# Performance work log

Measured on AMD Instinct MI355X. Metric: run time of the kernel, lower is better.

## Reference

```python
import jax, jax.numpy as jnp
import numpy as np

B, C, H, W = 4, 256, 128, 128
HEADS, KD, VD = 8, 64, 64
EPS = 1e-5


def setup_inputs() -> dict:
    key = jax.random.key(0)
    ks = jax.random.split(key, 5)
    s = 0.02
    return {
        "x": jax.random.normal(ks[0], (B, C, H, W), dtype=jnp.float32),
        "wq": jax.random.normal(ks[1], (HEADS * KD, C), dtype=jnp.float32) * s,
        "bq": jnp.zeros((HEADS * KD,), dtype=jnp.float32),
        "wk": jax.random.normal(ks[2], (HEADS * KD, C), dtype=jnp.float32) * s,
        "bk": jnp.zeros((HEADS * KD,), dtype=jnp.float32),
        "wv": jax.random.normal(ks[3], (HEADS * VD, C), dtype=jnp.float32) * s,
        "bv": jnp.zeros((HEADS * VD,), dtype=jnp.float32),
        "wo": jax.random.normal(ks[4], (C, HEADS * VD), dtype=jnp.float32) * s,
        "bo": jnp.zeros((C,), dtype=jnp.float32),
        "g_q": jnp.ones((KD,), dtype=jnp.float32),
        "be_q": jnp.zeros((KD,), dtype=jnp.float32),
        "g_k": jnp.ones((KD,), dtype=jnp.float32),
        "be_k": jnp.zeros((KD,), dtype=jnp.float32),
        "g_v": jnp.ones((VD,), dtype=jnp.float32),
        "be_v": jnp.zeros((VD,), dtype=jnp.float32),
    }


def _conv1x1(t, w, b):
    # t: [B,C,H,W], w: [O,C] -> [B,O,H,W]
    return jnp.einsum("bchw,oc->bohw", t, w) + b[None, :, None, None]


def _ln_dim(t, g, be):
    # LayerNorm over the per-head feature axis (axis=2) of [B,heads,dim,N]
    mu = jnp.mean(t, axis=2, keepdims=True)
    var = jnp.var(t, axis=2, keepdims=True)
    return (t - mu) * jax.lax.rsqrt(var + EPS) * g[None, None, :, None] + be[None, None, :, None]


def reference(x, wq, bq, wk, bk, wv, bv, wo, bo, g_q, be_q, g_k, be_k, g_v, be_v):
    b, c, h, w = x.shape
    n = h * w
    # context defaults to x
    q = _conv1x1(x, wq, bq).reshape(b, HEADS, KD, n)
    k = _conv1x1(x, wk, bk).reshape(b, HEADS, KD, n)
    v = _conv1x1(x, wv, bv).reshape(b, HEADS, VD, n)
    q = _ln_dim(q, g_q, be_q)
    k = _ln_dim(k, g_k, be_k)
    v = _ln_dim(v, g_v, be_v)
    q = jax.nn.softmax(q * (KD ** -0.25), axis=2)  # softmax over key_dim
    k = jax.nn.softmax(k, axis=3)                  # softmax over N
    ctx = jnp.einsum("bhkn,bhvn->bhkv", k, v)      # [B,heads,KD,VD]
    out = jnp.einsum("bhkn,bhkv->bhvn", q, ctx)    # [B,heads,VD,N]
    out = out.reshape(b, HEADS * VD, h, w)
    return _conv1x1(out, wo, bo)
```

## Files before the change

### kernel.cpp

```cpp
#include <hip/hip_runtime.h>
#include <hip/hip_bf16.h>
#include <stdint.h>

typedef unsigned short u16;
typedef __attribute__((__vector_size__(16))) short s16x8;
typedef __attribute__((__vector_size__(16))) float f32x4;

#define N_ 16384
#define C_ 256

__device__ __forceinline__ float bf2f(u16 u) {
    union { uint32_t i; float f; } v; v.i = ((uint32_t)u) << 16; return v.f;
}
__device__ __forceinline__ u16 f2bf(float f) {
    union { uint32_t i; float f; } v; v.f = f;
    uint32_t u = v.i;
    return (u16)((u + 0x7FFFu + ((u >> 16) & 1u)) >> 16);
}

__device__ __forceinline__ void gl_lds16(const u16* g, u16* l) {
    __builtin_amdgcn_global_load_lds((__attribute__((address_space(1))) void*)g,
                                     (__attribute__((address_space(3))) void*)l,
                                     16, 0, 0);
}

__global__ __launch_bounds__(256) void zero_kernel(float* __restrict__ p, int n) {
    int i = blockIdx.x * 256 + threadIdx.x;
    if (i < n) p[i] = 0.f;
}

__global__ __launch_bounds__(256) void transpose_kernel(const float* __restrict__ x,
                                                        u16* __restrict__ xT) {
    __shared__ float T[64][65];
    int tid = threadIdx.x;
    int n0 = blockIdx.x * 64, c0 = blockIdx.y * 64, b = blockIdx.z;
    const float* xp = x + (size_t)b * C_ * N_;
    for (int it = 0; it < 16; it++) {
        int idx = it * 256 + tid;
        int c = idx >> 6, n = idx & 63;
        T[c][n] = xp[(size_t)(c0 + c) * N_ + n0 + n];
    }
    __syncthreads();
    u16* op = xT + (size_t)b * N_ * C_;
    for (int it = 0; it < 8; it++) {
        int idx = it * 256 + tid;
        int n = idx >> 5, c2 = (idx & 31) * 2;
        uint32_t lo = f2bf(T[c2][n]);
        uint32_t hi = f2bf(T[c2 + 1][n]);
        *(uint32_t*)&op[(size_t)(n0 + n) * C_ + c0 + c2] = lo | (hi << 16);
    }
}

__global__ __launch_bounds__(256) void cvtw_kernel(const float* __restrict__ wq,
                                                   const float* __restrict__ wk,
                                                   const float* __restrict__ wv,
                                                   u16* __restrict__ wb) {
    int m = blockIdx.y;
    const float* s = m == 0 ? wq : (m == 1 ? wk : wv);
    int i = blockIdx.x * 256 + threadIdx.x;
    wb[(size_t)m * 131072 + i] = f2bf(s[i]);
}


__global__ __launch_bounds__(256) void kv_kernel(
    const u16* __restrict__ xT, const u16* __restrict__ wb,
    const float* __restrict__ bk, const float* __restrict__ bv,
    const float* __restrict__ gk, const float* __restrict__ bek,
    const float* __restrict__ gv, const float* __restrict__ bev,
    u16* __restrict__ eKb, u16* __restrict__ vbb, float* __restrict__ rs)
{
    __shared__ u16 WS[128 * 64];
    __shared__ u16 XS[128 * 64];
    int tid = threadIdx.x;
    int lane = tid & 63, wid = tid >> 6;
    int quad = lane >> 4, l15 = lane & 15;
    int wm = wid >> 1, wn = wid & 1;
    int bx = blockIdx.x, sec = blockIdx.y, b = blockIdx.z;
    int kind2 = sec >> 2, pair = sec & 3;
    int r0 = pair * 128;
    int n0 = bx * 128;

    const float* bptr  = kind2 ? bv  : bk;
    const float* gptr  = kind2 ? gv  : gk;
    const float* beptr = kind2 ? bev : bek;
    const u16* wsrc = wb + (size_t)(1 + kind2) * 131072 + (size_t)r0 * 256;
    const u16* xsrc = xT + ((size_t)b * N_ + n0) * 256;

    f32x4 acc[4][4];
#pragma unroll
    for (int i = 0; i < 4; i++)
#pragma unroll
        for (int j = 0; j < 4; j++) acc[i][j] = (f32x4){0.f, 0.f, 0.f, 0.f};

    int srow = lane >> 3;
    int sc8  = ((lane & 7) ^ srow) * 8;

    for (int kc = 0; kc < 4; kc++) {
        int koff = kc * 64 + sc8;
#pragma unroll
        for (int i = 0; i < 4; i++) {
            int row = (wid * 4 + i) * 8 + srow;
            gl_lds16(&wsrc[(size_t)row * 256 + koff], &WS[(wid * 4 + i) * 512]);
            gl_lds16(&xsrc[(size_t)row * 256 + koff], &XS[(wid * 4 + i) * 512]);
        }
        __syncthreads();
#pragma unroll
        for (int ks = 0; ks < 2; ks++) {
            int cc = ks * 4 + quad;
            s16x8 af[4], bf[4];
#pragma unroll
            for (int f = 0; f < 4; f++) {
                int ar = wn * 64 + f * 16 + l15;
                int br = wm * 64 + f * 16 + l15;
                af[f] = *(const s16x8*)&XS[ar * 64 + ((cc ^ (ar & 7)) * 8)];
                bf[f] = *(const s16x8*)&WS[br * 64 + ((cc ^ (br & 7)) * 8)];
            }
#pragma unroll
            for (int i = 0; i < 4; i++)
#pragma unroll
                for (int j = 0; j < 4; j++)
                    acc[i][j] = __builtin_amdgcn_mfma_f32_16x16x32_bf16(af[i], bf[j], acc[i][j], 0, 0, 0);
        }
        __syncthreads();
    }

    int head = pair * 2 + wm;
    float bB_[4], gB[4], eB[4];
#pragma unroll
    for (int nf = 0; nf < 4; nf++) {
        int rl = nf * 16 + l15;
        bB_[nf] = bptr[head * 64 + rl];
        gB[nf]  = gptr[rl];
        eB[nf]  = beptr[rl];
    }
#pragma unroll
    for (int mf = 0; mf < 4; mf++)
#pragma unroll
        for (int nf = 0; nf < 4; nf++)
#pragma unroll
            for (int r = 0; r < 4; r++) acc[mf][nf][r] += bB_[nf];
    float sa[4][4], sb[4][4];
#pragma unroll
    for (int mf = 0; mf < 4; mf++)
#pragma unroll
        for (int r = 0; r < 4; r++) {
            float s = 0.f, s2 = 0.f;
#pragma unroll
            for (int nf = 0; nf < 4; nf++) { float v = acc[mf][nf][r]; s += v; s2 += v * v; }
            sa[mf][r] = s; sb[mf][r] = s2;
        }
#pragma unroll
    for (int msk = 1; msk <= 8; msk <<= 1)
#pragma unroll
        for (int mf = 0; mf < 4; mf++)
#pragma unroll
            for (int r = 0; r < 4; r++) {
                sa[mf][r] += __shfl_xor(sa[mf][r], msk);
                sb[mf][r] += __shfl_xor(sb[mf][r], msk);
            }
#pragma unroll
    for (int mf = 0; mf < 4; mf++)
#pragma unroll
        for (int r = 0; r < 4; r++) {
            float mu = sa[mf][r] * (1.f / 64.f);
            float rstd = rsqrtf(sb[mf][r] * (1.f / 64.f) - mu * mu + 1e-5f);
#pragma unroll
            for (int nf = 0; nf < 4; nf++)
                acc[mf][nf][r] = (acc[mf][nf][r] - mu) * rstd * gB[nf] + eB[nf];
        }
    if (kind2 == 0) {
#pragma unroll
        for (int mf = 0; mf < 4; mf++)
#pragma unroll
            for (int nf = 0; nf < 4; nf++)
#pragma unroll
                for (int r = 0; r < 4; r++) acc[mf][nf][r] = __expf(acc[mf][nf][r]);
#pragma unroll
        for (int nf = 0; nf < 4; nf++) {
            float s = 0.f;
#pragma unroll
            for (int mf = 0; mf < 4; mf++)
#pragma unroll
                for (int r = 0; r < 4; r++) s += acc[mf][nf][r];
            s += __shfl_xor(s, 16); s += __shfl_xor(s, 32);
            if (quad == 0)
                atomicAdd(&rs[(size_t)b * 512 + head * 64 + nf * 16 + l15], s);
        }
    }
    u16* op = (kind2 == 0) ? eKb : vbb;
    size_t tb = ((size_t)((b * 8 + head) * 128 + bx)) * 8192;
#pragma unroll
    for (int mf = 0; mf < 4; mf++)
#pragma unroll
        for (int nf = 0; nf < 4; nf++) {
            int rh = nf * 16 + l15;
            int ln = wn * 64 + mf * 16 + quad * 4;
            int c  = ln >> 3;
            int off = rh * 128 + ((c ^ (rh & 15)) * 8) + (ln & 7);
            uint64_t w0 = (uint64_t)f2bf(acc[mf][nf][0]) | ((uint64_t)f2bf(acc[mf][nf][1]) << 16) |
                          ((uint64_t)f2bf(acc[mf][nf][2]) << 32) | ((uint64_t)f2bf(acc[mf][nf][3]) << 48);
            *(uint64_t*)&op[tb + off] = w0;
        }
}

__global__ __launch_bounds__(256) void q_kernel(
    const u16* __restrict__ xT, const u16* __restrict__ wb,
    const float* __restrict__ bq, const float* __restrict__ gq, const float* __restrict__ beq,
    u16* __restrict__ qT)
{
    __shared__ u16 WS[128 * 64];
    __shared__ u16 XS[128 * 64];
    int tid = threadIdx.x;
    int lane = tid & 63, wid = tid >> 6;
    int quad = lane >> 4, l15 = lane & 15;
    int wm = wid >> 1, wn = wid & 1;
    int bx = blockIdx.x, pair = blockIdx.y, b = blockIdx.z;
    int r0 = pair * 128;
    int n0 = bx * 128;

    const u16* wsrc = wb + (size_t)r0 * 256;
    const u16* xsrc = xT + ((size_t)b * N_ + n0) * 256;

    f32x4 acc[4][4];
#pragma unroll
    for (int i = 0; i < 4; i++)
#pragma unroll
        for (int j = 0; j < 4; j++) acc[i][j] = (f32x4){0.f, 0.f, 0.f, 0.f};

    int srow = lane >> 3;
    int sc8  = ((lane & 7) ^ srow) * 8;

    for (int kc = 0; kc < 4; kc++) {
        int koff = kc * 64 + sc8;
#pragma unroll
        for (int i = 0; i < 4; i++) {
            int row = (wid * 4 + i) * 8 + srow;
            gl_lds16(&wsrc[(size_t)row * 256 + koff], &WS[(wid * 4 + i) * 512]);
            gl_lds16(&xsrc[(size_t)row * 256 + koff], &XS[(wid * 4 + i) * 512]);
        }
        __syncthreads();
#pragma unroll
        for (int ks = 0; ks < 2; ks++) {
            int cc = ks * 4 + quad;
            s16x8 af[4], bf[4];
#pragma unroll
            for (int f = 0; f < 4; f++) {
                int ar = wm * 64 + f * 16 + l15;
                int br = wn * 64 + f * 16 + l15;
                af[f] = *(const s16x8*)&WS[ar * 64 + ((cc ^ (ar & 7)) * 8)];
                bf[f] = *(const s16x8*)&XS[br * 64 + ((cc ^ (br & 7)) * 8)];
            }
#pragma unroll
            for (int i = 0; i < 4; i++)
#pragma unroll
                for (int j = 0; j < 4; j++)
                    acc[i][j] = __builtin_amdgcn_mfma_f32_16x16x32_bf16(af[i], bf[j], acc[i][j], 0, 0, 0);
        }
        __syncthreads();
    }

    float bA[4][4], gA[4][4], eA[4][4];
#pragma unroll
    for (int mf = 0; mf < 4; mf++)
#pragma unroll
        for (int r = 0; r < 4; r++) {
            int rl = mf * 16 + quad * 4 + r;
            bA[mf][r] = bq[r0 + wm * 64 + rl];
            gA[mf][r] = gq[rl];
            eA[mf][r] = beq[rl];
        }
#pragma unroll
    for (int mf = 0; mf < 4; mf++)
#pragma unroll
        for (int nf = 0; nf < 4; nf++)
#pragma unroll
            for (int r = 0; r < 4; r++) acc[mf][nf][r] += bA[mf][r];
#pragma unroll
    for (int nf = 0; nf < 4; nf++) {
        float s = 0.f, s2 = 0.f;
#pragma unroll
        for (int mf = 0; mf < 4; mf++)
#pragma unroll
            for (int r = 0; r < 4; r++) { float v = acc[mf][nf][r]; s += v; s2 += v * v; }
        s  += __shfl_xor(s, 16);  s  += __shfl_xor(s, 32);
        s2 += __shfl_xor(s2, 16); s2 += __shfl_xor(s2, 32);
        float mu = s * (1.f / 64.f);
        float rstd = rsqrtf(s2 * (1.f / 64.f) - mu * mu + 1e-5f);
#pragma unroll
        for (int mf = 0; mf < 4; mf++)
#pragma unroll
            for (int r = 0; r < 4; r++)
                acc[mf][nf][r] = (acc[mf][nf][r] - mu) * rstd * gA[mf][r] + eA[mf][r];
    }
    const float s_q = 0.35355339059327373f;
#pragma unroll
    for (int nf = 0; nf < 4; nf++) {
        float m = -1e30f;
#pragma unroll
        for (int mf = 0; mf < 4; mf++)
#pragma unroll
            for (int r = 0; r < 4; r++) { acc[mf][nf][r] *= s_q; m = fmaxf(m, acc[mf][nf][r]); }
        m = fmaxf(m, __shfl_xor(m, 16)); m = fmaxf(m, __shfl_xor(m, 32));
        float d = 0.f;
#pragma unroll
        for (int mf = 0; mf < 4; mf++)
#pragma unroll
            for (int r = 0; r < 4; r++) { float e = __expf(acc[mf][nf][r] - m); acc[mf][nf][r] = e; d += e; }
        d += __shfl_xor(d, 16); d += __shfl_xor(d, 32);
        float inv = 1.f / d;
#pragma unroll
        for (int mf = 0; mf < 4; mf++)
#pragma unroll
            for (int r = 0; r < 4; r++) acc[mf][nf][r] *= inv;
    }
    u16* qp = qT + (size_t)b * N_ * 512;
#pragma unroll
    for (int mf = 0; mf < 4; mf++)
#pragma unroll
        for (int nf = 0; nf < 4; nf++) {
            int n = n0 + wn * 64 + nf * 16 + l15;
            int g0 = r0 + wm * 64 + mf * 16 + quad * 4;
            uint64_t w0 = (uint64_t)f2bf(acc[mf][nf][0]) | ((uint64_t)f2bf(acc[mf][nf][1]) << 16) |
                          ((uint64_t)f2bf(acc[mf][nf][2]) << 32) | ((uint64_t)f2bf(acc[mf][nf][3]) << 48);
            *(uint64_t*)&qp[(size_t)n * 512 + g0] = w0;
        }
}

__global__ __launch_bounds__(256) void ctx_kernel(
    const u16* __restrict__ eKb, const u16* __restrict__ vbb,
    float* __restrict__ ctx_acc)
{
    __shared__ u16 ES[64 * 128];
    __shared__ u16 VS[64 * 128];
    __shared__ float CTXS[64 * 66];
    int tid = threadIdx.x;
    int lane = tid & 63, wid = tid >> 6;
    int quad = lane >> 4, l15 = lane & 15;
    int ns = blockIdx.x, h = blockIdx.y, b = blockIdx.z;
    for (int i = tid; i < 64 * 66; i += 256) CTXS[i] = 0.f;
    size_t hb = (size_t)(b * 8 + h) * 128;
    f32x4 acc[4][4];
#pragma unroll
    for (int i = 0; i < 4; i++)
#pragma unroll
        for (int j = 0; j < 4; j++) acc[i][j] = (f32x4){0.f, 0.f, 0.f, 0.f};

    for (int t = 0; t < 8; t++) {
        size_t tb = (hb + ns * 8 + t) * 8192;
#pragma unroll
        for (int i = 0; i < 4; i++) {
            size_t g = tb + ((size_t)((wid * 4 + i) * 64) + lane) * 8;
            gl_lds16(&eKb[g], &ES[(wid * 4 + i) * 512]);
            gl_lds16(&vbb[g], &VS[(wid * 4 + i) * 512]);
        }
        __syncthreads();
        int cc = wid * 4 + quad;
        s16x8 af[4], bf[4];
#pragma unroll
        for (int f = 0; f < 4; f++) {
            int off = (f * 16 + l15) * 128 + ((cc ^ l15) * 8);
            af[f] = *(const s16x8*)&ES[off];
            bf[f] = *(const s16x8*)&VS[off];
        }
#pragma unroll
        for (int i = 0; i < 4; i++)
#pragma unroll
            for (int j = 0; j < 4; j++)
                acc[i][j] = __builtin_amdgcn_mfma_f32_16x16x32_bf16(af[i], bf[j], acc[i][j], 0, 0, 0);
        __syncthreads();
    }
#pragma unroll
    for (int mf = 0; mf < 4; mf++)
#pragma unroll
        for (int nf = 0; nf < 4; nf++)
#pragma unroll
            for (int r = 0; r < 4; r++) {
                int kd = mf * 16 + quad * 4 + r, vd = nf * 16 + l15;
                atomicAdd(&CTXS[kd * 66 + vd], acc[mf][nf][r]);
            }
    __syncthreads();
    size_t base = ((size_t)b * 8 + h) * 4096;
    for (int i = tid; i < 4096; i += 256)
        atomicAdd(&ctx_acc[base + i], CTXS[(i >> 6) * 66 + (i & 63)]);
}

__global__ __launch_bounds__(256) void weff_kernel(
    const float* __restrict__ ctx_acc, const float* __restrict__ rs,
    const float* __restrict__ wo, u16* __restrict__ Weffb)
{
    __shared__ float CT[16][65];
    int tid = threadIdx.x;
    int h = blockIdx.x, b = blockIdx.y, kc = blockIdx.z;
    for (int i = tid; i < 1024; i += 256) {
        int kdl = i >> 6, vd = i & 63;
        int kd = kc * 16 + kdl;
        CT[kdl][vd] = ctx_acc[(((size_t)b * 8 + h) * 64 + kd) * 64 + vd] /
                      rs[(size_t)b * 512 + h * 64 + kd];
    }
    __syncthreads();
    int c = tid;
    float wrow[64];
    const float4* wp = (const float4*)(wo + (size_t)c * 512 + h * 64);
#pragma unroll
    for (int i = 0; i < 16; i++) { float4 t = wp[i]; wrow[i*4] = t.x; wrow[i*4+1] = t.y; wrow[i*4+2] = t.z; wrow[i*4+3] = t.w; }
    for (int kdl = 0; kdl < 16; kdl++) {
        float s = 0.f;
#pragma unroll
        for (int vd = 0; vd < 64; vd++) s += wrow[vd] * CT[kdl][vd];
        Weffb[((size_t)b * 256 + c) * 512 + h * 64 + kc * 16 + kdl] = f2bf(s);
    }
}

__global__ __launch_bounds__(256) void out_kernel(
    const u16* __restrict__ Weffb, const u16* __restrict__ qT,
    const float* __restrict__ bo, float* __restrict__ out)
{
    __shared__ u16 WS[128 * 64];
    __shared__ u16 XS[128 * 64];
    int tid = threadIdx.x;
    int lane = tid & 63, wid = tid >> 6;
    int quad = lane >> 4, l15 = lane & 15;
    int wm = wid >> 1, wn = wid & 1;
    int n0 = blockIdx.x * 128, c0 = blockIdx.y * 128, b = blockIdx.z;
    const u16* asrc = Weffb + ((size_t)b * 256 + c0) * 512;
    const u16* bsrc = qT + ((size_t)b * N_ + n0) * 512;

    f32x4 acc[4][4];
#pragma unroll
    for (int i = 0; i < 4; i++)
#pragma unroll
        for (int j = 0; j < 4; j++) acc[i][j] = (f32x4){0.f, 0.f, 0.f, 0.f};

    int srow = lane >> 3;
    int sc8  = ((lane & 7) ^ srow) * 8;

    for (int kc = 0; kc < 8; kc++) {
        int koff = kc * 64 + sc8;
#pragma unroll
        for (int i = 0; i < 4; i++) {
            int row = (wid * 4 + i) * 8 + srow;
            gl_lds16(&asrc[(size_t)row * 512 + koff], &WS[(wid * 4 + i) * 512]);
            gl_lds16(&bsrc[(size_t)row * 512 + koff], &XS[(wid * 4 + i) * 512]);
        }
        __syncthreads();
#pragma unroll
        for (int ks = 0; ks < 2; ks++) {
            int cc = ks * 4 + quad;
            s16x8 af[4], bf[4];
#pragma unroll
            for (int f = 0; f < 4; f++) {
                int ar = wm * 64 + f * 16 + l15;
                int br = wn * 64 + f * 16 + l15;
                af[f] = *(const s16x8*)&WS[ar * 64 + ((cc ^ (ar & 7)) * 8)];
                bf[f] = *(const s16x8*)&XS[br * 64 + ((cc ^ (br & 7)) * 8)];
            }
#pragma unroll
            for (int i = 0; i < 4; i++)
#pragma unroll
                for (int j = 0; j < 4; j++)
                    acc[i][j] = __builtin_amdgcn_mfma_f32_16x16x32_bf16(af[i], bf[j], acc[i][j], 0, 0, 0);
        }
        __syncthreads();
    }
#pragma unroll
    for (int mf = 0; mf < 4; mf++)
#pragma unroll
        for (int r = 0; r < 4; r++) {
            int c = c0 + wm * 64 + mf * 16 + quad * 4 + r;
            float bov = bo[c];
#pragma unroll
            for (int nf = 0; nf < 4; nf++)
                out[((size_t)b * 256 + c) * N_ + n0 + wn * 64 + nf * 16 + l15] = acc[mf][nf][r] + bov;
        }
}

extern "C" void kernel_launch(void* const* d_in, const int* in_sizes, int n_in,
                              void* d_out, int out_size, void* d_ws, size_t ws_size,
                              hipStream_t stream) {
    const float* x   = (const float*)d_in[0];
    const float* wq  = (const float*)d_in[1];
    const float* bq  = (const float*)d_in[2];
    const float* wk  = (const float*)d_in[3];
    const float* bk  = (const float*)d_in[4];
    const float* wv  = (const float*)d_in[5];
    const float* bv  = (const float*)d_in[6];
    const float* wo  = (const float*)d_in[7];
    const float* bo  = (const float*)d_in[8];
    const float* gq  = (const float*)d_in[9];
    const float* beq = (const float*)d_in[10];
    const float* gk  = (const float*)d_in[11];
    const float* bek = (const float*)d_in[12];
    const float* gv  = (const float*)d_in[13];
    const float* bev = (const float*)d_in[14];
    float* out = (float*)d_out;

    char* ws = (char*)d_ws;
    u16* xT      = (u16*)(ws);
    u16* wb      = (u16*)(ws + 33554432ULL);
    u16* eKb     = (u16*)(ws + 34340864ULL);
    u16* qT      = (u16*)(ws + 34340864ULL);
    u16* vbb     = (u16*)(ws + 101449728ULL);
    float* ctx_a = (float*)(ws + 168558592ULL);
    float* rs    = (float*)(ws + 169082880ULL);
    u16* Weffb   = (u16*)(ws + 169091072ULL);

    cvtw_kernel<<<dim3(512, 3), 256, 0, stream>>>(wq, wk, wv, wb);
    transpose_kernel<<<dim3(256, 4, 4), 256, 0, stream>>>(x, xT);
    zero_kernel<<<dim3(520), 256, 0, stream>>>(ctx_a, 133120);

    kv_kernel<<<dim3(128, 8, 4), 256, 0, stream>>>(
        xT, wb, bk, bv, gk, bek, gv, bev, eKb, vbb, rs);

    ctx_kernel<<<dim3(16, 8, 4), 256, 0, stream>>>(eKb, vbb, ctx_a);

    q_kernel<<<dim3(128, 4, 4), 256, 0, stream>>>(xT, wb, bq, gq, beq, qT);

    weff_kernel<<<dim3(8, 4, 4), 256, 0, stream>>>(ctx_a, rs, wo, Weffb);

    out_kernel<<<dim3(128, 2, 4), 256, 0, stream>>>(Weffb, qT, bo, out);
}
```

Baseline: 382.1 us.

## Double-buffer LDS tiles in GEMM kernels and stage epilogue stores through LDS

Replaces the single WS/XS LDS buffers in kv, q and out kernels with a double-buffered array. The next K-chunk is issued via global_load_lds while MFMAs run on the current chunk, which also drops one barrier per iteration. The kv and q epilogues now write bf16 results into LDS first and then emit 16-byte coalesced global stores instead of scattered 8-byte stores. LDS use doubles to 64KB per block, which may lower occupancy. Correctness depends on the async LDS loads being complete at the single remaining barrier.

```diff
diff --git a/kernel.cpp b/kernel.cpp
--- a/kernel.cpp
+++ b/kernel.cpp
@@ -62,6 +62,15 @@
 }
 
 
+#define STAGE2(WSRC, XSRC, LDW, KC, CUR) {                                         \
+    int koff_ = (KC) * 64 + sc8;                                                   \
+    _Pragma("unroll")                                                              \
+    for (int i_ = 0; i_ < 4; i_++) {                                               \
+        int row_ = (wid * 4 + i_) * 8 + srow;                                      \
+        gl_lds16(&(WSRC)[(size_t)row_ * (LDW) + koff_], &SH[CUR][(wid * 4 + i_) * 512]);      \
+        gl_lds16(&(XSRC)[(size_t)row_ * (LDW) + koff_], &SH[2 + (CUR)][(wid * 4 + i_) * 512]); \
+    } }
+
 __global__ __launch_bounds__(256) void kv_kernel(
     const u16* __restrict__ xT, const u16* __restrict__ wb,
     const float* __restrict__ bk, const float* __restrict__ bv,
@@ -69,8 +78,7 @@
     const float* __restrict__ gv, const float* __restrict__ bev,
     u16* __restrict__ eKb, u16* __restrict__ vbb, float* __restrict__ rs)
 {
-    __shared__ u16 WS[128 * 64];
-    __shared__ u16 XS[128 * 64];
+    __shared__ u16 SH[4][8192];
     int tid = threadIdx.x;
     int lane = tid & 63, wid = tid >> 6;
     int quad = lane >> 4, l15 = lane & 15;
@@ -95,15 +103,13 @@
     int srow = lane >> 3;
     int sc8  = ((lane & 7) ^ srow) * 8;
 
+    STAGE2(wsrc, xsrc, 256, 0, 0);
+    __syncthreads();
     for (int kc = 0; kc < 4; kc++) {
-        int koff = kc * 64 + sc8;
-#pragma unroll
-        for (int i = 0; i < 4; i++) {
-            int row = (wid * 4 + i) * 8 + srow;
-            gl_lds16(&wsrc[(size_t)row * 256 + koff], &WS[(wid * 4 + i) * 512]);
-            gl_lds16(&xsrc[(size_t)row * 256 + koff], &XS[(wid * 4 + i) * 512]);
-        }
-        __syncthreads();
+        int cur = kc & 1;
+        if (kc < 3) STAGE2(wsrc, xsrc, 256, kc + 1, cur ^ 1);
+        const u16* Wb = &SH[cur][0];
+        const u16* Xb = &SH[2 + cur][0];
 #pragma unroll
         for (int ks = 0; ks < 2; ks++) {
             int cc = ks * 4 + quad;
@@ -112,8 +118,8 @@
             for (int f = 0; f < 4; f++) {
                 int ar = wn * 64 + f * 16 + l15;
                 int br = wm * 64 + f * 16 + l15;
-                af[f] = *(const s16x8*)&XS[ar * 64 + ((cc ^ (ar & 7)) * 8)];
-                bf[f] = *(const s16x8*)&WS[br * 64 + ((cc ^ (br & 7)) * 8)];
+                af[f] = *(const s16x8*)&Xb[ar * 64 + ((cc ^ (ar & 7)) * 8)];
+                bf[f] = *(const s16x8*)&Wb[br * 64 + ((cc ^ (br & 7)) * 8)];
             }
 #pragma unroll
             for (int i = 0; i < 4; i++)
@@ -121,7 +127,7 @@
                 for (int j = 0; j < 4; j++)
                     acc[i][j] = __builtin_amdgcn_mfma_f32_16x16x32_bf16(af[i], bf[j], acc[i][j], 0, 0, 0);
         }
-        __syncthreads();
+        if (kc < 3) __syncthreads();
     }
 
     int head = pair * 2 + wm;
@@ -188,7 +194,7 @@
         }
     }
     u16* op = (kind2 == 0) ? eKb : vbb;
-    size_t tb = ((size_t)((b * 8 + head) * 128 + bx)) * 8192;
+    u16* st = (wm == 0) ? &SH[0][0] : &SH[2][0];
 #pragma unroll
     for (int mf = 0; mf < 4; mf++)
 #pragma unroll
@@ -199,8 +205,20 @@
             int off = rh * 128 + ((c ^ (rh & 15)) * 8) + (ln & 7);
             uint64_t w0 = (uint64_t)f2bf(acc[mf][nf][0]) | ((uint64_t)f2bf(acc[mf][nf][1]) << 16) |
                           ((uint64_t)f2bf(acc[mf][nf][2]) << 32) | ((uint64_t)f2bf(acc[mf][nf][3]) << 48);
-            *(uint64_t*)&op[tb + off] = w0;
-        }
+            *(uint64_t*)&st[off] = w0;
+        }
+    __syncthreads();
+    {
+        int tile = tid >> 7, t = tid & 127;
+        const u16* src = (tile == 0) ? &SH[0][0] : &SH[2][0];
+        int headt = pair * 2 + tile;
+        size_t tb = ((size_t)((b * 8 + headt) * 128 + bx)) * 8192;
+#pragma unroll
+        for (int i = 0; i < 8; i++) {
+            int j = (i * 128 + t) * 8;
+            *(s16x8*)&op[tb + j] = *(const s16x8*)&src[j];
+        }
+    }
 }
 
 __global__ __launch_bounds__(256) void q_kernel(
@@ -208,8 +226,7 @@
     const float* __restrict__ bq, const float* __restrict__ gq, const float* __restrict__ beq,
     u16* __restrict__ qT)
 {
-    __shared__ u16 WS[128 * 64];
-    __shared__ u16 XS[128 * 64];
+    __shared__ u16 SH[4][8192];
     int tid = threadIdx.x;
     int lane = tid & 63, wid = tid >> 6;
     int quad = lane >> 4, l15 = lane & 15;
@@ -230,15 +247,13 @@
     int srow = lane >> 3;
     int sc8  = ((lane & 7) ^ srow) * 8;
 
+    STAGE2(wsrc, xsrc, 256, 0, 0);
+    __syncthreads();
     for (int kc = 0; kc < 4; kc++) {
-        int koff = kc * 64 + sc8;
-#pragma unroll
-        for (int i = 0; i < 4; i++) {
-            int row = (wid * 4 + i) * 8 + srow;
-            gl_lds16(&wsrc[(size_t)row * 256 + koff], &WS[(wid * 4 + i) * 512]);
-            gl_lds16(&xsrc[(size_t)row * 256 + koff], &XS[(wid * 4 + i) * 512]);
-        }
-        __syncthreads();
+        int cur = kc & 1;
+        if (kc < 3) STAGE2(wsrc, xsrc, 256, kc + 1, cur ^ 1);
+        const u16* Wb = &SH[cur][0];
+        const u16* Xb = &SH[2 + cur][0];
 #pragma unroll
         for (int ks = 0; ks < 2; ks++) {
             int cc = ks * 4 + quad;
@@ -247,8 +262,8 @@
             for (int f = 0; f < 4; f++) {
                 int ar = wm * 64 + f * 16 + l15;
                 int br = wn * 64 + f * 16 + l15;
-                af[f] = *(const s16x8*)&WS[ar * 64 + ((cc ^ (ar & 7)) * 8)];
-                bf[f] = *(const s16x8*)&XS[br * 64 + ((cc ^ (br & 7)) * 8)];
+                af[f] = *(const s16x8*)&Wb[ar * 64 + ((cc ^ (ar & 7)) * 8)];
+                bf[f] = *(const s16x8*)&Xb[br * 64 + ((cc ^ (br & 7)) * 8)];
             }
 #pragma unroll
             for (int i = 0; i < 4; i++)
@@ -256,7 +271,7 @@
                 for (int j = 0; j < 4; j++)
                     acc[i][j] = __builtin_amdgcn_mfma_f32_16x16x32_bf16(af[i], bf[j], acc[i][j], 0, 0, 0);
         }
-        __syncthreads();
+        if (kc < 3) __syncthreads();
     }
 
     float bA[4][4], gA[4][4], eA[4][4];
@@ -313,17 +328,32 @@
 #pragma unroll
             for (int r = 0; r < 4; r++) acc[mf][nf][r] *= inv;
     }
-    u16* qp = qT + (size_t)b * N_ * 512;
+    u16* st = (wn == 0) ? &SH[0][0] : &SH[2][0];
 #pragma unroll
     for (int mf = 0; mf < 4; mf++)
 #pragma unroll
         for (int nf = 0; nf < 4; nf++) {
-            int n = n0 + wn * 64 + nf * 16 + l15;
-            int g0 = r0 + wm * 64 + mf * 16 + quad * 4;
+            int nl = nf * 16 + l15;
+            int gl = wm * 64 + mf * 16 + quad * 4;
+            int c  = gl >> 3;
+            int off = nl * 128 + ((c ^ (nl & 15)) * 8) + (gl & 7);
             uint64_t w0 = (uint64_t)f2bf(acc[mf][nf][0]) | ((uint64_t)f2bf(acc[mf][nf][1]) << 16) |
                           ((uint64_t)f2bf(acc[mf][nf][2]) << 32) | ((uint64_t)f2bf(acc[mf][nf][3]) << 48);
-            *(uint64_t*)&qp[(size_t)n * 512 + g0] = w0;
-        }
+            *(uint64_t*)&st[off] = w0;
+        }
+    __syncthreads();
+    {
+        u16* qp = qT + (size_t)b * N_ * 512;
+#pragma unroll
+        for (int i = 0; i < 8; i++) {
+            int idx = i * 256 + tid;
+            int n = idx >> 4, cp = idx & 15;
+            const u16* src = (n < 64) ? &SH[0][0] : &SH[2][0];
+            int nl = n & 63;
+            s16x8 v = *(const s16x8*)&src[nl * 128 + ((cp ^ (nl & 15)) * 8)];
+            *(s16x8*)&qp[(size_t)(n0 + n) * 512 + r0 + cp * 8] = v;
+        }
+    }
 }
 
 __global__ __launch_bounds__(256) void ctx_kernel(
@@ -415,8 +445,7 @@
     const u16* __restrict__ Weffb, const u16* __restrict__ qT,
     const float* __restrict__ bo, float* __restrict__ out)
 {
-    __shared__ u16 WS[128 * 64];
-    __shared__ u16 XS[128 * 64];
+    __shared__ u16 SH[4][8192];
     int tid = threadIdx.x;
     int lane = tid & 63, wid = tid >> 6;
     int quad = lane >> 4, l15 = lane & 15;
@@ -434,15 +463,13 @@
     int srow = lane >> 3;
     int sc8  = ((lane & 7) ^ srow) * 8;
 
+    STAGE2(asrc, bsrc, 512, 0, 0);
+    __syncthreads();
     for (int kc = 0; kc < 8; kc++) {
-        int koff = kc * 64 + sc8;
-#pragma unroll
-        for (int i = 0; i < 4; i++) {
-            int row = (wid * 4 + i) * 8 + srow;
-            gl_lds16(&asrc[(size_t)row * 512 + koff], &WS[(wid * 4 + i) * 512]);
-            gl_lds16(&bsrc[(size_t)row * 512 + koff], &XS[(wid * 4 + i) * 512]);
-        }
-        __syncthreads();
+        int cur = kc & 1;
+        if (kc < 7) STAGE2(asrc, bsrc, 512, kc + 1, cur ^ 1);
+        const u16* Wb = &SH[cur][0];
+        const u16* Xb = &SH[2 + cur][0];
 #pragma unroll
         for (int ks = 0; ks < 2; ks++) {
             int cc = ks * 4 + quad;
@@ -451,8 +478,8 @@
             for (int f = 0; f < 4; f++) {
                 int ar = wm * 64 + f * 16 + l15;
                 int br = wn * 64 + f * 16 + l15;
-                af[f] = *(const s16x8*)&WS[ar * 64 + ((cc ^ (ar & 7)) * 8)];
-                bf[f] = *(const s16x8*)&XS[br * 64 + ((cc ^ (br & 7)) * 8)];
+                af[f] = *(const s16x8*)&Wb[ar * 64 + ((cc ^ (ar & 7)) * 8)];
+                bf[f] = *(const s16x8*)&Xb[br * 64 + ((cc ^ (br & 7)) * 8)];
             }
 #pragma unroll
             for (int i = 0; i < 4; i++)
@@ -460,7 +487,7 @@
                 for (int j = 0; j < 4; j++)
                     acc[i][j] = __builtin_amdgcn_mfma_f32_16x16x32_bf16(af[i], bf[j], acc[i][j], 0, 0, 0);
         }
-        __syncthreads();
+        if (kc < 7) __syncthreads();
     }
 #pragma unroll
     for (int mf = 0; mf < 4; mf++)
```

Result: no change. 380.3 us (-0.5%).

## Give each wave private LDS tiles to drop block-wide barriers in GEMM kernels

Applied to the files above, without the earlier changes.

The three MFMA GEMM kernels (q, kv, out) now have each wave load its own 64-row slices of both operands into a private LDS region. The block-wide __syncthreads calls are replaced by a per-wave vmcnt wait and scheduling barriers. This removes cross-wave synchronisation stalls, but it doubles global-to-LDS traffic because operand tiles are no longer shared between waves. LDS use per block also doubles to 64 KB, which can lower occupancy.

```diff
diff --git a/kernel.cpp b/kernel.cpp
--- a/kernel.cpp
+++ b/kernel.cpp
@@ -69,8 +69,7 @@
     const float* __restrict__ gv, const float* __restrict__ bev,
     u16* __restrict__ eKb, u16* __restrict__ vbb, float* __restrict__ rs)
 {
-    __shared__ u16 WS[128 * 64];
-    __shared__ u16 XS[128 * 64];
+    __shared__ u16 SH[4][8192];
     int tid = threadIdx.x;
     int lane = tid & 63, wid = tid >> 6;
     int quad = lane >> 4, l15 = lane & 15;
@@ -83,8 +82,11 @@
     const float* bptr  = kind2 ? bv  : bk;
     const float* gptr  = kind2 ? gv  : gk;
     const float* beptr = kind2 ? bev : bek;
-    const u16* wsrc = wb + (size_t)(1 + kind2) * 131072 + (size_t)r0 * 256;
-    const u16* xsrc = xT + ((size_t)b * N_ + n0) * 256;
+    const u16* wsrc = wb + (size_t)(1 + kind2) * 131072 + (size_t)(r0 + wm * 64) * 256;
+    const u16* xsrc = xT + ((size_t)b * N_ + n0 + wn * 64) * 256;
+
+    u16* Wl = &SH[wid][0];
+    u16* Xl = &SH[wid][4096];
 
     f32x4 acc[4][4];
 #pragma unroll
@@ -98,22 +100,23 @@
     for (int kc = 0; kc < 4; kc++) {
         int koff = kc * 64 + sc8;
 #pragma unroll
-        for (int i = 0; i < 4; i++) {
-            int row = (wid * 4 + i) * 8 + srow;
-            gl_lds16(&wsrc[(size_t)row * 256 + koff], &WS[(wid * 4 + i) * 512]);
-            gl_lds16(&xsrc[(size_t)row * 256 + koff], &XS[(wid * 4 + i) * 512]);
-        }
-        __syncthreads();
+        for (int i = 0; i < 8; i++) {
+            int row = i * 8 + srow;
+            gl_lds16(&wsrc[(size_t)row * 256 + koff], &Wl[i * 512]);
+            gl_lds16(&xsrc[(size_t)row * 256 + koff], &Xl[i * 512]);
+        }
+        asm volatile("s_waitcnt vmcnt(0)" ::: "memory");
+        __builtin_amdgcn_sched_barrier(0);
 #pragma unroll
         for (int ks = 0; ks < 2; ks++) {
             int cc = ks * 4 + quad;
             s16x8 af[4], bf[4];
 #pragma unroll
             for (int f = 0; f < 4; f++) {
-                int ar = wn * 64 + f * 16 + l15;
-                int br = wm * 64 + f * 16 + l15;
-                af[f] = *(const s16x8*)&XS[ar * 64 + ((cc ^ (ar & 7)) * 8)];
-                bf[f] = *(const s16x8*)&WS[br * 64 + ((cc ^ (br & 7)) * 8)];
+                int r = f * 16 + l15;
+                int sw = (cc ^ (r & 7)) * 8;
+                af[f] = *(const s16x8*)&Xl[r * 64 + sw];
+                bf[f] = *(const s16x8*)&Wl[r * 64 + sw];
             }
 #pragma unroll
             for (int i = 0; i < 4; i++)
@@ -121,7 +124,7 @@
                 for (int j = 0; j < 4; j++)
                     acc[i][j] = __builtin_amdgcn_mfma_f32_16x16x32_bf16(af[i], bf[j], acc[i][j], 0, 0, 0);
         }
-        __syncthreads();
+        __builtin_amdgcn_sched_barrier(0);
     }
 
     int head = pair * 2 + wm;
@@ -208,8 +211,7 @@
     const float* __restrict__ bq, const float* __restrict__ gq, const float* __restrict__ beq,
     u16* __restrict__ qT)
 {
-    __shared__ u16 WS[128 * 64];
-    __shared__ u16 XS[128 * 64];
+    __shared__ u16 SH[4][8192];
     int tid = threadIdx.x;
     int lane = tid & 63, wid = tid >> 6;
     int quad = lane >> 4, l15 = lane & 15;
@@ -218,8 +220,11 @@
     int r0 = pair * 128;
     int n0 = bx * 128;
 
-    const u16* wsrc = wb + (size_t)r0 * 256;
-    const u16* xsrc = xT + ((size_t)b * N_ + n0) * 256;
+    const u16* wsrc = wb + (size_t)(r0 + wm * 64) * 256;
+    const u16* xsrc = xT + ((size_t)b * N_ + n0 + wn * 64) * 256;
+
+    u16* Wl = &SH[wid][0];
+    u16* Xl = &SH[wid][4096];
 
     f32x4 acc[4][4];
 #pragma unroll
@@ -233,22 +238,23 @@
     for (int kc = 0; kc < 4; kc++) {
         int koff = kc * 64 + sc8;
 #pragma unroll
-        for (int i = 0; i < 4; i++) {
-            int row = (wid * 4 + i) * 8 + srow;
-            gl_lds16(&wsrc[(size_t)row * 256 + koff], &WS[(wid * 4 + i) * 512]);
-            gl_lds16(&xsrc[(size_t)row * 256 + koff], &XS[(wid * 4 + i) * 512]);
-        }
-        __syncthreads();
+        for (int i = 0; i < 8; i++) {
+            int row = i * 8 + srow;
+            gl_lds16(&wsrc[(size_t)row * 256 + koff], &Wl[i * 512]);
+            gl_lds16(&xsrc[(size_t)row * 256 + koff], &Xl[i * 512]);
+        }
+        asm volatile("s_waitcnt vmcnt(0)" ::: "memory");
+        __builtin_amdgcn_sched_barrier(0);
 #pragma unroll
         for (int ks = 0; ks < 2; ks++) {
             int cc = ks * 4 + quad;
             s16x8 af[4], bf[4];
 #pragma unroll
             for (int f = 0; f < 4; f++) {
-                int ar = wm * 64 + f * 16 + l15;
-                int br = wn * 64 + f * 16 + l15;
-                af[f] = *(const s16x8*)&WS[ar * 64 + ((cc ^ (ar & 7)) * 8)];
-                bf[f] = *(const s16x8*)&XS[br * 64 + ((cc ^ (br & 7)) * 8)];
+                int r = f * 16 + l15;
+                int sw = (cc ^ (r & 7)) * 8;
+                af[f] = *(const s16x8*)&Wl[r * 64 + sw];
+                bf[f] = *(const s16x8*)&Xl[r * 64 + sw];
             }
 #pragma unroll
             for (int i = 0; i < 4; i++)
@@ -256,7 +262,7 @@
                 for (int j = 0; j < 4; j++)
                     acc[i][j] = __builtin_amdgcn_mfma_f32_16x16x32_bf16(af[i], bf[j], acc[i][j], 0, 0, 0);
         }
-        __syncthreads();
+        __builtin_amdgcn_sched_barrier(0);
     }
 
     float bA[4][4], gA[4][4], eA[4][4];
@@ -415,15 +421,17 @@
     const u16* __restrict__ Weffb, const u16* __restrict__ qT,
     const float* __restrict__ bo, float* __restrict__ out)
 {
-    __shared__ u16 WS[128 * 64];
-    __shared__ u16 XS[128 * 64];
+    __shared__ u16 SH[4][8192];
     int tid = threadIdx.x;
     int lane = tid & 63, wid = tid >> 6;
     int quad = lane >> 4, l15 = lane & 15;
     int wm = wid >> 1, wn = wid & 1;
     int n0 = blockIdx.x * 128, c0 = blockIdx.y * 128, b = blockIdx.z;
-    const u16* asrc = Weffb + ((size_t)b * 256 + c0) * 512;
-    const u16* bsrc = qT + ((size_t)b * N_ + n0) * 512;
+    const u16* asrc = Weffb + ((size_t)b * 256 + c0 + wm * 64) * 512;
+    const u16* bsrc = qT + ((size_t)b * N_ + n0 + wn * 64) * 512;
+
+    u16* Wl = &SH[wid][0];
+    u16* Xl = &SH[wid][4096];
 
     f32x4 acc[4][4];
 #pragma unroll
@@ -437,22 +445,23 @@
     for (int kc = 0; kc < 8; kc++) {
         int koff = kc * 64 + sc8;
 #pragma unroll
-        for (int i = 0; i < 4; i++) {
-            int row = (wid * 4 + i) * 8 + srow;
-            gl_lds16(&asrc[(size_t)row * 512 + koff], &WS[(wid * 4 + i) * 512]);
-            gl_lds16(&bsrc[(size_t)row * 512 + koff], &XS[(wid * 4 + i) * 512]);
-        }
-        __syncthreads();
+        for (int i = 0; i < 8; i++) {
+            int row = i * 8 + srow;
+            gl_lds16(&asrc[(size_t)row * 512 + koff], &Wl[i * 512]);
+            gl_lds16(&bsrc[(size_t)row * 512 + koff], &Xl[i * 512]);
+        }
+        asm volatile("s_waitcnt vmcnt(0)" ::: "memory");
+        __builtin_amdgcn_sched_barrier(0);
 #pragma unroll
         for (int ks = 0; ks < 2; ks++) {
             int cc = ks * 4 + quad;
             s16x8 af[4], bf[4];
 #pragma unroll
             for (int f = 0; f < 4; f++) {
-                int ar = wm * 64 + f * 16 + l15;
-                int br = wn * 64 + f * 16 + l15;
-                af[f] = *(const s16x8*)&WS[ar * 64 + ((cc ^ (ar & 7)) * 8)];
-                bf[f] = *(const s16x8*)&XS[br * 64 + ((cc ^ (br & 7)) * 8)];
+                int r = f * 16 + l15;
+                int sw = (cc ^ (r & 7)) * 8;
+                af[f] = *(const s16x8*)&Wl[r * 64 + sw];
+                bf[f] = *(const s16x8*)&Xl[r * 64 + sw];
             }
 #pragma unroll
             for (int i = 0; i < 4; i++)
@@ -460,7 +469,7 @@
                 for (int j = 0; j < 4; j++)
                     acc[i][j] = __builtin_amdgcn_mfma_f32_16x16x32_bf16(af[i], bf[j], acc[i][j], 0, 0, 0);
         }
-        __syncthreads();
+        __builtin_amdgcn_sched_barrier(0);
     }
 #pragma unroll
     for (int mf = 0; mf < 4; mf++)
```

Result: no change. 385.1 us (+0.8%).
